# Kernel optimization log

Hardware: AMD Instinct MI355X
Metric: run time of the kernel (lower is better)

## Reference

```python
import jax, jax.numpy as jnp
import numpy as np

# Module hyperparameters (init_kwargs)
OUTLINER_RATIO = 0.01
SUB_RATIO = 0.2
SUB_BIT = 8
RANK = 16


def setup_inputs() -> dict:
    key = jax.random.key(0)
    x = jax.random.normal(key, (8, 2048, 4096), dtype=jnp.float32)
    return {"x": x}


def _lowrank_approx(A, q, key):
    """Randomized rank-q approximation of A (torch.svd_lowrank style, niter=2).
    A: [N, D]. Returns Q @ (Q^T A), a rank-q approximation of A."""
    n = A.shape[1]
    omega = jax.random.normal(key, (n, q), dtype=A.dtype)
    Q, _ = jnp.linalg.qr(A @ omega)            # [N, q]
    for _ in range(2):                          # power iterations
        Q2, _ = jnp.linalg.qr(A.T @ Q)          # [D, q]
        Q, _ = jnp.linalg.qr(A @ Q2)            # [N, q]
    return Q @ (Q.T @ A)                        # [N, D], rank q


def _get_statistics(x):
    """Outlier threshold (1-ratio quantile of |x[0]|), top-norm column list,
    and per-tensor symmetric quantization scale for the sub-outlier columns."""
    ax0 = jnp.abs(x[0]).ravel()
    k = int(ax0.shape[0] * (1.0 - OUTLINER_RATIO))      # kthvalue, 1-indexed
    outliner = jnp.sort(ax0)[k - 1]
    col_norm = jnp.mean(jnp.abs(x), axis=(0, 1))        # [D] per-column mean |x|
    kcols = int(x.shape[-1] * SUB_RATIO)
    _, cols = jax.lax.top_k(col_norm, kcols)            # sub-outlier column ids
    col_mask = jnp.zeros((x.shape[-1],), bool).at[cols].set(True)
    x_rem = jnp.where(jnp.abs(x) > outliner, 0.0, x)    # remove outliers
    x_sub = jnp.where(col_mask, x_rem, 0.0)
    qmax = float(2 ** (SUB_BIT - 1) - 1)
    scale = jnp.max(jnp.abs(x_sub)) / qmax
    return outliner, cols, scale


def _compress(x, outliner, cols, scale):
    """fake_divide_outliner_suboutlinear_svd: split x into outliers (kept exact),
    sub-outlier columns (fake-quantized to SUB_BIT bits), and a rank-RANK
    approximation of the remainder; recombine."""
    shape = x.shape
    D = shape[-1]
    x_out = jnp.where(jnp.abs(x) > outliner, x, 0.0)
    x_rem = x - x_out
    col_mask = jnp.zeros((D,), bool).at[cols].set(True)
    x_sub = jnp.where(col_mask, x_rem, 0.0)
    x_rem2 = x_rem - x_sub
    qmax = 2 ** (SUB_BIT - 1) - 1
    x_sub_q = jnp.clip(jnp.round(x_sub / scale), -qmax - 1, qmax) * scale
    x_lr = _lowrank_approx(x_rem2.reshape(-1, D), RANK, jax.random.key(42))
    return x_lr.reshape(shape) + x_out + x_sub_q


def reference(x):
    # forward output of the module is exact-erf GELU (F.gelu default)
    result = jax.nn.gelu(x, approximate=False)
    # iteration=0 < 10: compute statistics and the compressed activation
    # that would be saved for backward (this is the custom-kernel-heavy path).
    outliner, cols, scale = _get_statistics(x)
    x_compressed = _compress(x, outliner, cols, scale)
    return result, x_compressed, outliner, scale
```

## Files before the change

kernel.cpp:

```cpp
#include <hip/hip_runtime.h>
#include <math.h>

#define D_   4096
#define N_   16384
#define TOT  67108864ULL
#define KSEL 8304721u

__device__ unsigned long long g_colsum[D_];
__device__ unsigned int  g_hist[2048];
__device__ unsigned int  g_state[2];
__device__ float         g_outliner;
__device__ unsigned int  g_maxbits;
__device__ float         g_scale;
__device__ unsigned char g_mask[D_];
__device__ float g_omega[D_ * 16];
__device__ float g_tall [N_ * 16];
__device__ float g_small[D_ * 16];
__device__ float g_part [16777216];
__device__ float g_gpart[256 * 256];
__device__ float g_M[256];

__device__ __forceinline__ unsigned rotl32(unsigned v, int s) { return (v << s) | (v >> (32 - s)); }

__device__ __forceinline__ float erfinv32(float xx) {
  float w = -log1pf(-xx * xx);
  float p;
  if (w < 5.f) {
    w -= 2.5f;
    p = 2.81022636e-08f;
    p = fmaf(p, w, 3.43273939e-07f);
    p = fmaf(p, w, -3.5233877e-06f);
    p = fmaf(p, w, -4.39150654e-06f);
    p = fmaf(p, w, 0.00021858087f);
    p = fmaf(p, w, -0.00125372503f);
    p = fmaf(p, w, -0.00417768164f);
    p = fmaf(p, w, 0.246640727f);
    p = fmaf(p, w, 1.50140941f);
  } else {
    w = sqrtf(w) - 3.f;
    p = -0.000200214257f;
    p = fmaf(p, w, 0.000100950558f);
    p = fmaf(p, w, 0.00134934322f);
    p = fmaf(p, w, -0.00367342844f);
    p = fmaf(p, w, 0.00573950773f);
    p = fmaf(p, w, -0.0076224613f);
    p = fmaf(p, w, 0.00943887047f);
    p = fmaf(p, w, 1.00167406f);
    p = fmaf(p, w, 2.83297682f);
  }
  return p * xx;
}

__device__ __forceinline__ float bits_to_normal(unsigned b) {
  float f = __uint_as_float((b >> 9) | 0x3f800000u) - 1.0f;
  float u = fmaf(f, 2.0f, -0.99999994f);
  u = fmaxf(-0.99999994f, u);
  return 1.41421356f * erfinv32(u);
}

__device__ __forceinline__ float gelu_exact(float v) {
  return 0.5f * v * (1.f + erff(v * 0.70710678f));
}

__global__ void k_init() {
  int t = threadIdx.x;
  for (int i = t; i < D_; i += 256) g_colsum[i] = 0ull;
  for (int i = t; i < 2048; i += 256) g_hist[i] = 0u;
  if (t == 0) { g_state[0] = KSEL; g_state[1] = 0u; g_maxbits = 0u; }
}

__global__ __launch_bounds__(256) void k_pass1(const float* __restrict__ x, float* __restrict__ out0) {
  __shared__ unsigned lh[4 * 2056];
  int t = threadIdx.x, b = blockIdx.x;
  bool doh = (b < 64);
  for (int i = t; i < 4 * 2056; i += 256) lh[i] = 0u;
  int cp = (t >> 6) * 2056;
  float acc[16];
#pragma unroll
  for (int j = 0; j < 16; ++j) acc[j] = 0.f;
  __syncthreads();
  const float4* xv = (const float4*)(x + (size_t)b * 131072);
  float4* ov = (float4*)(out0 + (size_t)b * 131072);
  for (int i = 0; i < 128; i += 4) {
#pragma unroll
    for (int jj = 0; jj < 4; ++jj) {
      int f = t + 256 * (i + jj);
      float4 v = xv[f];
      float4 g;
      g.x = gelu_exact(v.x); g.y = gelu_exact(v.y); g.z = gelu_exact(v.z); g.w = gelu_exact(v.w);
      ov[f] = g;
      acc[jj * 4 + 0] += fabsf(v.x);
      acc[jj * 4 + 1] += fabsf(v.y);
      acc[jj * 4 + 2] += fabsf(v.z);
      acc[jj * 4 + 3] += fabsf(v.w);
      if (doh) {
        atomicAdd(&lh[cp + ((__float_as_uint(v.x) & 0x7fffffffu) >> 21)], 1u);
        atomicAdd(&lh[cp + ((__float_as_uint(v.y) & 0x7fffffffu) >> 21)], 1u);
        atomicAdd(&lh[cp + ((__float_as_uint(v.z) & 0x7fffffffu) >> 21)], 1u);
        atomicAdd(&lh[cp + ((__float_as_uint(v.w) & 0x7fffffffu) >> 21)], 1u);
      }
    }
  }
#pragma unroll
  for (int jj = 0; jj < 4; ++jj) {
    int c4 = t + 256 * jj;
#pragma unroll
    for (int k = 0; k < 4; ++k) {
      unsigned long long q = (unsigned long long)((double)acc[jj * 4 + k] * 4294967296.0 + 0.5);
      atomicAdd(&g_colsum[4 * c4 + k], q);
    }
  }
  if (doh) {
    __syncthreads();
    for (int i = t; i < 2048; i += 256) {
      unsigned c = lh[i] + lh[2056 + i] + lh[4112 + i] + lh[6168 + i];
      if (c) atomicAdd(&g_hist[i], c);
    }
  }
}

__global__ __launch_bounds__(256) void k_histL(const float* __restrict__ x, int level) {
  __shared__ unsigned lh[2048];
  int t = threadIdx.x, b = blockIdx.x;
  for (int i = t; i < 2048; i += 256) lh[i] = 0u;
  __syncthreads();
  unsigned pre = g_state[1];
  const float4* xv = (const float4*)x;
  size_t base = (size_t)b * 16384;
  for (int i = 0; i < 64; ++i) {
    float4 v = xv[base + t + 256 * i];
    unsigned u;
#define HPROC(comp) \
    u = __float_as_uint(comp) & 0x7fffffffu; \
    if (level == 1) { if ((u >> 21) == (pre >> 21)) atomicAdd(&lh[(u >> 10) & 0x7ffu], 1u); } \
    else            { if ((u >> 10) == (pre >> 10)) atomicAdd(&lh[u & 0x3ffu], 1u); }
    HPROC(v.x) HPROC(v.y) HPROC(v.z) HPROC(v.w)
#undef HPROC
  }
  __syncthreads();
  for (int i = t; i < 2048; i += 256) { unsigned c = lh[i]; if (c) atomicAdd(&g_hist[i], c); }
}

__global__ void k_scan(int level, float* __restrict__ od) {
  __shared__ unsigned h[2048];
  __shared__ unsigned ps[256];
  int t = threadIdx.x;
  unsigned loc = 0;
#pragma unroll
  for (int i = 0; i < 8; ++i) { unsigned v = g_hist[t * 8 + i]; h[t * 8 + i] = v; loc += v; }
  ps[t] = loc;
  __syncthreads();
  if (t == 0) {
    unsigned krem = g_state[0], pre = g_state[1];
    unsigned cum = 0; int g = 0;
    for (; g < 255; ++g) { if (cum + ps[g] >= krem) break; cum += ps[g]; }
    int b = g * 8;
    for (; b < 2047; ++b) { if (cum + h[b] >= krem) break; cum += h[b]; }
    krem -= cum;
    if (level == 0)      pre = ((unsigned)b) << 21;
    else if (level == 1) pre |= ((unsigned)b) << 10;
    else { pre |= (unsigned)b; g_outliner = __uint_as_float(pre); od[0] = __uint_as_float(pre); }
    g_state[0] = krem; g_state[1] = pre;
  }
  __syncthreads();
  for (int i = t; i < 2048; i += 256) g_hist[i] = 0u;
}

__global__ __launch_bounds__(1024) void k_colsel() {
  __shared__ unsigned long long s[4096];
  int t = threadIdx.x;
  for (int m = 0; m < 4; ++m) s[t + 1024 * m] = g_colsum[t + 1024 * m];
  __syncthreads();
  for (int k = 2; k <= 4096; k <<= 1) {
    for (int j = k >> 1; j > 0; j >>= 1) {
#pragma unroll
      for (int m = 0; m < 4; ++m) {
        int i = t + 1024 * m;
        int l = i ^ j;
        if (l > i) {
          unsigned long long a = s[i], c = s[l];
          bool up = ((i & k) == 0);
          if (up ? (a > c) : (a < c)) { s[i] = c; s[l] = a; }
        }
      }
      __syncthreads();
    }
  }
  unsigned long long T = s[4096 - 819];
  for (int m = 0; m < 4; ++m) { int i = t + 1024 * m; g_mask[i] = (g_colsum[i] >= T) ? 1 : 0; }
}

__global__ void k_omega() {
  unsigned i = blockIdx.x * 256 + threadIdx.x;
  if (i >= 65536u) return;
  const unsigned ks0 = 0u, ks1 = 42u, ks2 = 0x1BD11BDAu ^ 42u;
  unsigned x0 = 0u + ks0;
  unsigned x1 = i  + ks1;
#define RND(r) { x0 += x1; x1 = rotl32(x1, r); x1 ^= x0; }
  RND(13) RND(15) RND(26) RND(6)   x0 += ks1; x1 += ks2 + 1u;
  RND(17) RND(29) RND(16) RND(24)  x0 += ks2; x1 += ks0 + 2u;
  RND(13) RND(15) RND(26) RND(6)   x0 += ks0; x1 += ks1 + 3u;
  RND(17) RND(29) RND(16) RND(24)  x0 += ks1; x1 += ks2 + 4u;
  RND(13) RND(15) RND(26) RND(6)   x0 += ks2; x1 += ks0 + 5u;
#undef RND
  g_omega[i] = bits_to_normal(x0 ^ x1);
}

__global__ __launch_bounds__(256) void k_AB(const float* __restrict__ x, int bsel) {
  __shared__ float xt[256 * 33];
  int t = threadIdx.x;
  int rb = blockIdx.x, ks = blockIdx.y;
  const float* Bm = bsel ? g_small : g_omega;
  float thr = g_outliner;
  float acc[16];
#pragma unroll
  for (int q = 0; q < 16; ++q) acc[q] = 0.f;
  int row0 = rb * 256;
  for (int ch = 0; ch < 8; ++ch) {
    int d0 = ks * 256 + ch * 32;
#pragma unroll
    for (int m = 0; m < 8; ++m) {
      int f = t + 256 * m;
      int r = f >> 3, c4 = f & 7;
      float4 v = *(const float4*)(x + (size_t)(row0 + r) * D_ + d0 + 4 * c4);
      uchar4 mk = *(const uchar4*)(g_mask + d0 + 4 * c4);
      float a0 = (mk.x || fabsf(v.x) > thr) ? 0.f : v.x;
      float a1 = (mk.y || fabsf(v.y) > thr) ? 0.f : v.y;
      float a2 = (mk.z || fabsf(v.z) > thr) ? 0.f : v.z;
      float a3 = (mk.w || fabsf(v.w) > thr) ? 0.f : v.w;
      int base = r * 33 + 4 * c4;
      xt[base + 0] = a0; xt[base + 1] = a1; xt[base + 2] = a2; xt[base + 3] = a3;
    }
    __syncthreads();
    for (int d = 0; d < 32; ++d) {
      const float* br = Bm + (size_t)(d0 + d) * 16;
      float a0 = xt[t * 33 + d];
#pragma unroll
      for (int q = 0; q < 16; ++q) acc[q] = fmaf(a0, br[q], acc[q]);
    }
    __syncthreads();
  }
  float* p0 = g_part + ((size_t)ks * N_ + row0 + t) * 16;
#pragma unroll
  for (int q4 = 0; q4 < 4; ++q4)
    *(float4*)(p0 + 4 * q4) = make_float4(acc[4*q4], acc[4*q4+1], acc[4*q4+2], acc[4*q4+3]);
}

__global__ __launch_bounds__(1024) void k_AtB(const float* __restrict__ x, int do_max) {
  __shared__ float wm[16];
  int t = threadIdx.x, b = blockIdx.x;
  float thr = g_outliner;
  uchar4 mk = *(const uchar4*)(g_mask + 4 * t);
  float acc[4][16];
#pragma unroll
  for (int j = 0; j < 4; ++j)
#pragma unroll
    for (int q = 0; q < 16; ++q) acc[j][q] = 0.f;
  float mx = 0.f;
  size_t row0 = (size_t)b * 64;
  for (int r = 0; r < 64; ++r) {
    size_t row = row0 + r;
    float4 v = *(const float4*)(x + row * D_ + 4 * t);
    const float* br = g_tall + row * 16;
    float ax = fabsf(v.x), ay = fabsf(v.y), az = fabsf(v.z), aw = fabsf(v.w);
    float a0 = (mk.x || ax > thr) ? 0.f : v.x;
    float a1 = (mk.y || ay > thr) ? 0.f : v.y;
    float a2 = (mk.z || az > thr) ? 0.f : v.z;
    float a3 = (mk.w || aw > thr) ? 0.f : v.w;
    if (do_max) {
      if (mk.x && ax <= thr) mx = fmaxf(mx, ax);
      if (mk.y && ay <= thr) mx = fmaxf(mx, ay);
      if (mk.z && az <= thr) mx = fmaxf(mx, az);
      if (mk.w && aw <= thr) mx = fmaxf(mx, aw);
    }
#pragma unroll
    for (int q = 0; q < 16; ++q) {
      float bq = br[q];
      acc[0][q] = fmaf(a0, bq, acc[0][q]);
      acc[1][q] = fmaf(a1, bq, acc[1][q]);
      acc[2][q] = fmaf(a2, bq, acc[2][q]);
      acc[3][q] = fmaf(a3, bq, acc[3][q]);
    }
  }
  float* pb = g_part + ((size_t)b * D_ + 4 * t) * 16;
#pragma unroll
  for (int j = 0; j < 4; ++j)
#pragma unroll
    for (int q4 = 0; q4 < 4; ++q4)
      *(float4*)(pb + j * 16 + 4 * q4) =
        make_float4(acc[j][4*q4], acc[j][4*q4+1], acc[j][4*q4+2], acc[j][4*q4+3]);
  if (do_max) {
#pragma unroll
    for (int off = 32; off > 0; off >>= 1) mx = fmaxf(mx, __shfl_xor(mx, off, 64));
    if ((t & 63) == 0) wm[t >> 6] = mx;
    __syncthreads();
    if (t == 0) {
      float m2 = wm[0];
      for (int i = 1; i < 16; ++i) m2 = fmaxf(m2, wm[i]);
      atomicMax(&g_maxbits, __float_as_uint(m2));
    }
  }
}

__global__ __launch_bounds__(256) void k_combG0() {
  __shared__ float ys[1024];
  int t = threadIdx.x, blk = blockIdx.x;
#pragma unroll
  for (int m = 0; m < 4; ++m) {
    int j = blk * 1024 + m * 256 + t;
    float s = 0.f;
    for (int k2 = 0; k2 < 16; ++k2) s += g_part[k2 * 262144 + j];
    g_tall[j] = s;
    ys[m * 256 + t] = s;
  }
  __syncthreads();
  int a = t >> 4, b = t & 15;
  float acc = 0.f;
  for (int r = 0; r < 64; ++r) acc = fmaf(ys[r * 16 + a], ys[r * 16 + b], acc);
  g_gpart[blk * 256 + t] = acc;
}

__global__ __launch_bounds__(256) void k_combG1(int do_scale, float* __restrict__ od) {
  __shared__ float ys[256];
  int t = threadIdx.x, blk = blockIdx.x;
  int j = blk * 256 + t;
  float s = 0.f;
  for (int k2 = 0; k2 < 256; ++k2) s += g_part[k2 * 65536 + j];
  g_small[j] = s;
  ys[t] = s;
  if (do_scale && blk == 0 && t == 0) {
    float sc = __uint_as_float(g_maxbits) / 127.0f;
    g_scale = sc; od[0] = sc;
  }
  __syncthreads();
  int a = t >> 4, b = t & 15;
  float acc = 0.f;
  for (int r = 0; r < 16; ++r) acc = fmaf(ys[r * 16 + a], ys[r * 16 + b], acc);
  g_gpart[blk * 256 + t] = acc;
}

__global__ void k_chol(int mode) {
  __shared__ double G[256], L[256], M[256];
  int t = threadIdx.x;
  double s = 0.0;
  for (int p = 0; p < 256; ++p) s += (double)g_gpart[p * 256 + t];
  G[t] = s; M[t] = 0.0; L[t] = 0.0;
  __syncthreads();
  for (int j = 0; j < 16; ++j) {
    if (t == j) {
      double d = G[j * 16 + j];
      for (int k = 0; k < j; ++k) d -= L[j * 16 + k] * L[j * 16 + k];
      L[j * 16 + j] = sqrt(d);
    }
    __syncthreads();
    if (t > j && t < 16) {
      double d = G[t * 16 + j];
      for (int k = 0; k < j; ++k) d -= L[t * 16 + k] * L[j * 16 + k];
      L[t * 16 + j] = d / L[j * 16 + j];
    }
    __syncthreads();
  }
  if (t < 16) {
    int jc = t;
    M[jc * 16 + jc] = 1.0 / L[jc * 16 + jc];
    for (int i2 = jc + 1; i2 < 16; ++i2) {
      double s2 = 0.0;
      for (int k = jc; k < i2; ++k) s2 += L[i2 * 16 + k] * M[k * 16 + jc];
      M[i2 * 16 + jc] = -s2 / L[i2 * 16 + i2];
    }
  }
  __syncthreads();
  if (mode == 0) g_M[t] = (float)M[t];
  else {
    int i2 = t >> 4, j2 = t & 15;
    double s2 = 0.0;
    for (int k = 0; k < 16; ++k) s2 += M[k * 16 + i2] * M[k * 16 + j2];
    g_M[t] = (float)s2;
  }
}

__global__ __launch_bounds__(256) void k_scaleQ(int which) {
  __shared__ float Mf[256];
  float* Y = which ? g_small : g_tall;
  int t = threadIdx.x;
  Mf[t] = g_M[t];
  __syncthreads();
  size_t row = (size_t)blockIdx.x * 256 + t;
  float4* yr = (float4*)(Y + row * 16);
  float4 v0 = yr[0], v1 = yr[1], v2 = yr[2], v3 = yr[3];
  float y[16] = {v0.x,v0.y,v0.z,v0.w, v1.x,v1.y,v1.z,v1.w, v2.x,v2.y,v2.z,v2.w, v3.x,v3.y,v3.z,v3.w};
  float q[16];
#pragma unroll
  for (int jq = 0; jq < 16; ++jq) {
    float s = 0.f;
    for (int iq = 0; iq <= jq; ++iq) s = fmaf(Mf[jq * 16 + iq], y[iq], s);
    q[jq] = s;
  }
  yr[0] = make_float4(q[0],q[1],q[2],q[3]);
  yr[1] = make_float4(q[4],q[5],q[6],q[7]);
  yr[2] = make_float4(q[8],q[9],q[10],q[11]);
  yr[3] = make_float4(q[12],q[13],q[14],q[15]);
}

__global__ __launch_bounds__(256) void k_Zsolve() {
  __shared__ float Gf[256];
  int t = threadIdx.x;
  Gf[t] = g_M[t];
  __syncthreads();
  size_t d = (size_t)blockIdx.x * 256 + t;
  float4* wr = (float4*)(g_small + d * 16);
  float4 v0 = wr[0], v1 = wr[1], v2 = wr[2], v3 = wr[3];
  float w[16] = {v0.x,v0.y,v0.z,v0.w, v1.x,v1.y,v1.z,v1.w, v2.x,v2.y,v2.z,v2.w, v3.x,v3.y,v3.z,v3.w};
  float z[16];
#pragma unroll
  for (int jq = 0; jq < 16; ++jq) {
    float s = 0.f;
#pragma unroll
    for (int iq = 0; iq < 16; ++iq) s = fmaf(Gf[jq * 16 + iq], w[iq], s);
    z[jq] = s;
  }
  wr[0] = make_float4(z[0],z[1],z[2],z[3]);
  wr[1] = make_float4(z[4],z[5],z[6],z[7]);
  wr[2] = make_float4(z[8],z[9],z[10],z[11]);
  wr[3] = make_float4(z[12],z[13],z[14],z[15]);
}

__global__ __launch_bounds__(256) void k_final(const float* __restrict__ x, float* __restrict__ out1) {
  __shared__ float zt[16 * 516];
  int t = threadIdx.x;
  int rb = blockIdx.x, pn = blockIdx.y;
  int d0 = pn * 512;
  int row0 = rb * 256;
#pragma unroll
  for (int i = 0; i < 8; ++i) {
    int f = t + 256 * i;
    int dd = f >> 2, q4 = f & 3;
    float4 zv = *(const float4*)(g_small + (size_t)(d0 + dd) * 16 + 4 * q4);
    zt[(4 * q4 + 0) * 516 + dd] = zv.x;
    zt[(4 * q4 + 1) * 516 + dd] = zv.y;
    zt[(4 * q4 + 2) * 516 + dd] = zv.z;
    zt[(4 * q4 + 3) * 516 + dd] = zv.w;
  }
  __syncthreads();
  float thr = g_outliner, sc = g_scale;
  int lf = t & 127;
  int half = t >> 7;
  int dl = 4 * lf;
  float4 zq[16];
#pragma unroll
  for (int q = 0; q < 16; ++q) zq[q] = *(const float4*)&zt[q * 516 + dl];
  uchar4 mk = *(const uchar4*)(g_mask + d0 + dl);
  for (int i = 0; i < 128; ++i) {
    int row = row0 + 2 * i + half;
    int rowu = __builtin_amdgcn_readfirstlane(row);
    const float* yr = g_tall + (size_t)rowu * 16;
    float4 v = *(const float4*)(x + (size_t)rowu * D_ + d0 + dl);
    float4 a = make_float4(0.f, 0.f, 0.f, 0.f);
#pragma unroll
    for (int q = 0; q < 16; ++q) {
      float yq = yr[q];
      a.x = fmaf(yq, zq[q].x, a.x); a.y = fmaf(yq, zq[q].y, a.y);
      a.z = fmaf(yq, zq[q].z, a.z); a.w = fmaf(yq, zq[q].w, a.w);
    }
    float4 o;
    o.x = a.x + (fabsf(v.x) > thr ? v.x : (mk.x ? fminf(fmaxf(rintf(v.x / sc), -128.f), 127.f) * sc : 0.f));
    o.y = a.y + (fabsf(v.y) > thr ? v.y : (mk.y ? fminf(fmaxf(rintf(v.y / sc), -128.f), 127.f) * sc : 0.f));
    o.z = a.z + (fabsf(v.z) > thr ? v.z : (mk.z ? fminf(fmaxf(rintf(v.z / sc), -128.f), 127.f) * sc : 0.f));
    o.w = a.w + (fabsf(v.w) > thr ? v.w : (mk.w ? fminf(fmaxf(rintf(v.w / sc), -128.f), 127.f) * sc : 0.f));
    *(float4*)(out1 + (size_t)rowu * D_ + d0 + dl) = o;
  }
}

extern "C" void kernel_launch(void* const* d_in, const int* in_sizes, int n_in,
                              void* d_out, int out_size, void* d_ws, size_t ws_size,
                              hipStream_t stream) {
  (void)in_sizes; (void)n_in; (void)out_size; (void)d_ws; (void)ws_size;
  const float* x = (const float*)d_in[0];
  float* out = (float*)d_out;
  float* out0    = out;
  float* out1    = out + TOT;
  float* o_outl  = out + 2 * TOT;
  float* o_scale = out + 2 * TOT + 1;

  hipLaunchKernelGGL(k_init,  dim3(1),   dim3(256), 0, stream);
  hipLaunchKernelGGL(k_pass1, dim3(512), dim3(256), 0, stream, x, out0);
  hipLaunchKernelGGL(k_scan,  dim3(1),   dim3(256), 0, stream, 0, o_outl);
  hipLaunchKernelGGL(k_histL, dim3(128), dim3(256), 0, stream, x, 1);
  hipLaunchKernelGGL(k_scan,  dim3(1),   dim3(256), 0, stream, 1, o_outl);
  hipLaunchKernelGGL(k_histL, dim3(128), dim3(256), 0, stream, x, 2);
  hipLaunchKernelGGL(k_scan,  dim3(1),   dim3(256), 0, stream, 2, o_outl);
  hipLaunchKernelGGL(k_colsel, dim3(1),  dim3(1024), 0, stream);
  hipLaunchKernelGGL(k_omega, dim3(256), dim3(256), 0, stream);
  hipLaunchKernelGGL(k_AB,     dim3(64, 16), dim3(256), 0, stream, x, 0);
  hipLaunchKernelGGL(k_combG0, dim3(256),    dim3(256), 0, stream);
  hipLaunchKernelGGL(k_chol,   dim3(1),      dim3(256), 0, stream, 0);
  hipLaunchKernelGGL(k_scaleQ, dim3(64),     dim3(256), 0, stream, 0);
  hipLaunchKernelGGL(k_AtB,    dim3(256), dim3(1024), 0, stream, x, 1);
  hipLaunchKernelGGL(k_combG1, dim3(256), dim3(256),  0, stream, 1, o_scale);
  hipLaunchKernelGGL(k_chol,   dim3(1),   dim3(256),  0, stream, 0);
  hipLaunchKernelGGL(k_scaleQ, dim3(16),  dim3(256),  0, stream, 1);
  hipLaunchKernelGGL(k_AB,     dim3(64, 16), dim3(256), 0, stream, x, 1);
  hipLaunchKernelGGL(k_combG0, dim3(256),    dim3(256), 0, stream);
  hipLaunchKernelGGL(k_chol,   dim3(1),      dim3(256), 0, stream, 0);
  hipLaunchKernelGGL(k_scaleQ, dim3(64),     dim3(256), 0, stream, 0);
  hipLaunchKernelGGL(k_AtB,    dim3(256), dim3(1024), 0, stream, x, 0);
  hipLaunchKernelGGL(k_combG1, dim3(256), dim3(256),  0, stream, 0, o_scale);
  hipLaunchKernelGGL(k_chol,   dim3(1),   dim3(256),  0, stream, 0);
  hipLaunchKernelGGL(k_scaleQ, dim3(16),  dim3(256),  0, stream, 1);
  hipLaunchKernelGGL(k_AB,     dim3(64, 16), dim3(256), 0, stream, x, 1);
  hipLaunchKernelGGL(k_combG0, dim3(256),    dim3(256), 0, stream);
  hipLaunchKernelGGL(k_chol,   dim3(1),      dim3(256), 0, stream, 1);
  hipLaunchKernelGGL(k_AtB,    dim3(256), dim3(1024), 0, stream, x, 0);
  hipLaunchKernelGGL(k_combG1, dim3(256), dim3(256),  0, stream, 0, o_scale);
  hipLaunchKernelGGL(k_Zsolve, dim3(16),  dim3(256),  0, stream);
  hipLaunchKernelGGL(k_final,  dim3(64, 8), dim3(256), 0, stream, x, out1);
}
```

Baseline: 1.086 ms.

## Cache masked residual matrix in fp16 for power-iteration passes

The first A·omega pass now writes the masked residual (outliers and sub-outlier columns zeroed) as an fp16 copy. Every later A·B and Aᵀ·B pass reads that half-size buffer instead of re-reading fp32 x and re-applying the mask. The sub-outlier max reduction moves into the first pass, and the scale is written in the following combine kernel. This halves the bytes read in six of the seven large streaming passes, at the cost of an extra 128MB write and fp16 rounding of the residual fed into the low-rank factorisation.

```diff
diff --git a/kernel.cpp b/kernel.cpp
--- a/kernel.cpp
+++ b/kernel.cpp
@@ -1,4 +1,5 @@
 #include <hip/hip_runtime.h>
+#include <hip/hip_fp16.h>
 #include <math.h>
 
 #define D_   4096
@@ -13,6 +14,7 @@
 __device__ unsigned int  g_maxbits;
 __device__ float         g_scale;
 __device__ unsigned char g_mask[D_];
+__device__ __half g_af16[N_ * (size_t)D_];
 __device__ float g_omega[D_ * 16];
 __device__ float g_tall [N_ * 16];
 __device__ float g_small[D_ * 16];
@@ -206,30 +208,60 @@
   g_omega[i] = bits_to_normal(x0 ^ x1);
 }
 
-__global__ __launch_bounds__(256) void k_AB(const float* __restrict__ x, int bsel) {
+__global__ __launch_bounds__(256) void k_AB(const float* __restrict__ x, int bsel, int stage1) {
   __shared__ float xt[256 * 33];
   int t = threadIdx.x;
   int rb = blockIdx.x, ks = blockIdx.y;
   const float* Bm = bsel ? g_small : g_omega;
   float thr = g_outliner;
+  float mx = 0.f;
   float acc[16];
 #pragma unroll
   for (int q = 0; q < 16; ++q) acc[q] = 0.f;
   int row0 = rb * 256;
   for (int ch = 0; ch < 8; ++ch) {
     int d0 = ks * 256 + ch * 32;
-#pragma unroll
-    for (int m = 0; m < 8; ++m) {
-      int f = t + 256 * m;
-      int r = f >> 3, c4 = f & 7;
-      float4 v = *(const float4*)(x + (size_t)(row0 + r) * D_ + d0 + 4 * c4);
-      uchar4 mk = *(const uchar4*)(g_mask + d0 + 4 * c4);
-      float a0 = (mk.x || fabsf(v.x) > thr) ? 0.f : v.x;
-      float a1 = (mk.y || fabsf(v.y) > thr) ? 0.f : v.y;
-      float a2 = (mk.z || fabsf(v.z) > thr) ? 0.f : v.z;
-      float a3 = (mk.w || fabsf(v.w) > thr) ? 0.f : v.w;
-      int base = r * 33 + 4 * c4;
-      xt[base + 0] = a0; xt[base + 1] = a1; xt[base + 2] = a2; xt[base + 3] = a3;
+    if (stage1) {
+#pragma unroll
+      for (int m = 0; m < 8; ++m) {
+        int f = t + 256 * m;
+        int r = f >> 3, c4 = f & 7;
+        size_t off = (size_t)(row0 + r) * D_ + d0 + 4 * c4;
+        float4 v = *(const float4*)(x + off);
+        uchar4 mk = *(const uchar4*)(g_mask + d0 + 4 * c4);
+        float ax = fabsf(v.x), ay = fabsf(v.y), az = fabsf(v.z), aw = fabsf(v.w);
+        float a0 = (mk.x || ax > thr) ? 0.f : v.x;
+        float a1 = (mk.y || ay > thr) ? 0.f : v.y;
+        float a2 = (mk.z || az > thr) ? 0.f : v.z;
+        float a3 = (mk.w || aw > thr) ? 0.f : v.w;
+        if (mk.x && ax <= thr) mx = fmaxf(mx, ax);
+        if (mk.y && ay <= thr) mx = fmaxf(mx, ay);
+        if (mk.z && az <= thr) mx = fmaxf(mx, az);
+        if (mk.w && aw <= thr) mx = fmaxf(mx, aw);
+        union { __half2 h2[2]; uint2 u; } pk;
+        pk.h2[0] = __floats2half2_rn(a0, a1);
+        pk.h2[1] = __floats2half2_rn(a2, a3);
+        *(uint2*)(&g_af16[off]) = pk.u;
+        int base = r * 33 + 4 * c4;
+        xt[base + 0] = a0; xt[base + 1] = a1; xt[base + 2] = a2; xt[base + 3] = a3;
+      }
+    } else {
+#pragma unroll
+      for (int m = 0; m < 4; ++m) {
+        int f = t + 256 * m;
+        int r = f >> 2, c8 = f & 3;
+        size_t off = (size_t)(row0 + r) * D_ + d0 + 8 * c8;
+        uint4 raw = *(const uint4*)(&g_af16[off]);
+        float2 f0 = __half22float2(*(__half2*)&raw.x);
+        float2 f1 = __half22float2(*(__half2*)&raw.y);
+        float2 f2 = __half22float2(*(__half2*)&raw.z);
+        float2 f3 = __half22float2(*(__half2*)&raw.w);
+        int base = r * 33 + 8 * c8;
+        xt[base + 0] = f0.x; xt[base + 1] = f0.y;
+        xt[base + 2] = f1.x; xt[base + 3] = f1.y;
+        xt[base + 4] = f2.x; xt[base + 5] = f2.y;
+        xt[base + 6] = f3.x; xt[base + 7] = f3.y;
+      }
     }
     __syncthreads();
     for (int d = 0; d < 32; ++d) {
@@ -244,42 +276,34 @@
 #pragma unroll
   for (int q4 = 0; q4 < 4; ++q4)
     *(float4*)(p0 + 4 * q4) = make_float4(acc[4*q4], acc[4*q4+1], acc[4*q4+2], acc[4*q4+3]);
-}
-
-__global__ __launch_bounds__(1024) void k_AtB(const float* __restrict__ x, int do_max) {
-  __shared__ float wm[16];
+  if (stage1) {
+#pragma unroll
+    for (int off = 32; off > 0; off >>= 1) mx = fmaxf(mx, __shfl_xor(mx, off, 64));
+    if ((t & 63) == 0) atomicMax(&g_maxbits, __float_as_uint(mx));
+  }
+}
+
+__global__ __launch_bounds__(1024) void k_AtB() {
   int t = threadIdx.x, b = blockIdx.x;
-  float thr = g_outliner;
-  uchar4 mk = *(const uchar4*)(g_mask + 4 * t);
   float acc[4][16];
 #pragma unroll
   for (int j = 0; j < 4; ++j)
 #pragma unroll
     for (int q = 0; q < 16; ++q) acc[j][q] = 0.f;
-  float mx = 0.f;
   size_t row0 = (size_t)b * 64;
   for (int r = 0; r < 64; ++r) {
     size_t row = row0 + r;
-    float4 v = *(const float4*)(x + row * D_ + 4 * t);
+    uint2 raw = *(const uint2*)(&g_af16[row * D_ + 4 * t]);
+    float2 f01 = __half22float2(*(__half2*)&raw.x);
+    float2 f23 = __half22float2(*(__half2*)&raw.y);
     const float* br = g_tall + row * 16;
-    float ax = fabsf(v.x), ay = fabsf(v.y), az = fabsf(v.z), aw = fabsf(v.w);
-    float a0 = (mk.x || ax > thr) ? 0.f : v.x;
-    float a1 = (mk.y || ay > thr) ? 0.f : v.y;
-    float a2 = (mk.z || az > thr) ? 0.f : v.z;
-    float a3 = (mk.w || aw > thr) ? 0.f : v.w;
-    if (do_max) {
-      if (mk.x && ax <= thr) mx = fmaxf(mx, ax);
-      if (mk.y && ay <= thr) mx = fmaxf(mx, ay);
-      if (mk.z && az <= thr) mx = fmaxf(mx, az);
-      if (mk.w && aw <= thr) mx = fmaxf(mx, aw);
-    }
 #pragma unroll
     for (int q = 0; q < 16; ++q) {
       float bq = br[q];
-      acc[0][q] = fmaf(a0, bq, acc[0][q]);
-      acc[1][q] = fmaf(a1, bq, acc[1][q]);
-      acc[2][q] = fmaf(a2, bq, acc[2][q]);
-      acc[3][q] = fmaf(a3, bq, acc[3][q]);
+      acc[0][q] = fmaf(f01.x, bq, acc[0][q]);
+      acc[1][q] = fmaf(f01.y, bq, acc[1][q]);
+      acc[2][q] = fmaf(f23.x, bq, acc[2][q]);
+      acc[3][q] = fmaf(f23.y, bq, acc[3][q]);
     }
   }
   float* pb = g_part + ((size_t)b * D_ + 4 * t) * 16;
@@ -289,22 +313,15 @@
     for (int q4 = 0; q4 < 4; ++q4)
       *(float4*)(pb + j * 16 + 4 * q4) =
         make_float4(acc[j][4*q4], acc[j][4*q4+1], acc[j][4*q4+2], acc[j][4*q4+3]);
-  if (do_max) {
-#pragma unroll
-    for (int off = 32; off > 0; off >>= 1) mx = fmaxf(mx, __shfl_xor(mx, off, 64));
-    if ((t & 63) == 0) wm[t >> 6] = mx;
-    __syncthreads();
-    if (t == 0) {
-      float m2 = wm[0];
-      for (int i = 1; i < 16; ++i) m2 = fmaxf(m2, wm[i]);
-      atomicMax(&g_maxbits, __float_as_uint(m2));
-    }
-  }
-}
-
-__global__ __launch_bounds__(256) void k_combG0() {
+}
+
+__global__ __launch_bounds__(256) void k_combG0(int do_scale, float* __restrict__ od) {
   __shared__ float ys[1024];
   int t = threadIdx.x, blk = blockIdx.x;
+  if (do_scale && blk == 0 && t == 0) {
+    float sc = __uint_as_float(g_maxbits) / 127.0f;
+    g_scale = sc; od[0] = sc;
+  }
 #pragma unroll
   for (int m = 0; m < 4; ++m) {
     int j = blk * 1024 + m * 256 + t;
@@ -320,7 +337,7 @@
   g_gpart[blk * 256 + t] = acc;
 }
 
-__global__ __launch_bounds__(256) void k_combG1(int do_scale, float* __restrict__ od) {
+__global__ __launch_bounds__(256) void k_combG1() {
   __shared__ float ys[256];
   int t = threadIdx.x, blk = blockIdx.x;
   int j = blk * 256 + t;
@@ -328,10 +345,6 @@
   for (int k2 = 0; k2 < 256; ++k2) s += g_part[k2 * 65536 + j];
   g_small[j] = s;
   ys[t] = s;
-  if (do_scale && blk == 0 && t == 0) {
-    float sc = __uint_as_float(g_maxbits) / 127.0f;
-    g_scale = sc; od[0] = sc;
-  }
   __syncthreads();
   int a = t >> 4, b = t & 15;
   float acc = 0.f;
@@ -491,27 +504,27 @@
   hipLaunchKernelGGL(k_scan,  dim3(1),   dim3(256), 0, stream, 2, o_outl);
   hipLaunchKernelGGL(k_colsel, dim3(1),  dim3(1024), 0, stream);
   hipLaunchKernelGGL(k_omega, dim3(256), dim3(256), 0, stream);
-  hipLaunchKernelGGL(k_AB,     dim3(64, 16), dim3(256), 0, stream, x, 0);
-  hipLaunchKernelGGL(k_combG0, dim3(256),    dim3(256), 0, stream);
+  hipLaunchKernelGGL(k_AB,     dim3(64, 16), dim3(256), 0, stream, x, 0, 1);
+  hipLaunchKernelGGL(k_combG0, dim3(256),    dim3(256), 0, stream, 1, o_scale);
   hipLaunchKernelGGL(k_chol,   dim3(1),      dim3(256), 0, stream, 0);
   hipLaunchKernelGGL(k_scaleQ, dim3(64),     dim3(256), 0, stream, 0);
-  hipLaunchKernelGGL(k_AtB,    dim3(256), dim3(1024), 0, stream, x, 1);
-  hipLaunchKernelGGL(k_combG1, dim3(256), dim3(256),  0, stream, 1, o_scale);
+  hipLaunchKernelGGL(k_AtB,    dim3(256), dim3(1024), 0, stream);
+  hipLaunchKernelGGL(k_combG1, dim3(256), dim3(256),  0, stream);
   hipLaunchKernelGGL(k_chol,   dim3(1),   dim3(256),  0, stream, 0);
   hipLaunchKernelGGL(k_scaleQ, dim3(16),  dim3(256),  0, stream, 1);
-  hipLaunchKernelGGL(k_AB,     dim3(64, 16), dim3(256), 0, stream, x, 1);
-  hipLaunchKernelGGL(k_combG0, dim3(256),    dim3(256), 0, stream);
+  hipLaunchKernelGGL(k_AB,     dim3(64, 16), dim3(256), 0, stream, x, 1, 0);
+  hipLaunchKernelGGL(k_combG0, dim3(256),    dim3(256), 0, stream, 0, o_scale);
   hipLaunchKernelGGL(k_chol,   dim3(1),      dim3(256), 0, stream, 0);
   hipLaunchKernelGGL(k_scaleQ, dim3(64),     dim3(256), 0, stream, 0);
-  hipLaunchKernelGGL(k_AtB,    dim3(256), dim3(1024), 0, stream, x, 0);
-  hipLaunchKernelGGL(k_combG1, dim3(256), dim3(256),  0, stream, 0, o_scale);
+  hipLaunchKernelGGL(k_AtB,    dim3(256), dim3(1024), 0, stream);
+  hipLaunchKernelGGL(k_combG1, dim3(256), dim3(256),  0, stream);
   hipLaunchKernelGGL(k_chol,   dim3(1),   dim3(256),  0, stream, 0);
   hipLaunchKernelGGL(k_scaleQ, dim3(16),  dim3(256),  0, stream, 1);
-  hipLaunchKernelGGL(k_AB,     dim3(64, 16), dim3(256), 0, stream, x, 1);
-  hipLaunchKernelGGL(k_combG0, dim3(256),    dim3(256), 0, stream);
+  hipLaunchKernelGGL(k_AB,     dim3(64, 16), dim3(256), 0, stream, x, 1, 0);
+  hipLaunchKernelGGL(k_combG0, dim3(256),    dim3(256), 0, stream, 0, o_scale);
   hipLaunchKernelGGL(k_chol,   dim3(1),      dim3(256), 0, stream, 1);
-  hipLaunchKernelGGL(k_AtB,    dim3(256), dim3(1024), 0, stream, x, 0);
-  hipLaunchKernelGGL(k_combG1, dim3(256), dim3(256),  0, stream, 0, o_scale);
+  hipLaunchKernelGGL(k_AtB,    dim3(256), dim3(1024), 0, stream);
+  hipLaunchKernelGGL(k_combG1, dim3(256), dim3(256),  0, stream);
   hipLaunchKernelGGL(k_Zsolve, dim3(16),  dim3(256),  0, stream);
   hipLaunchKernelGGL(k_final,  dim3(64, 8), dim3(256), 0, stream, x, out1);
 }
```

New measurement: 1.123 ms. 3.4% more time.

## Fuse small reduction, Cholesky and scaling kernels using grid-wide atomic barriers

Applied to the files above, without the earlier changes.

Merges the column-combine, Gram, Cholesky, Q-scaling and Z-solve launches into the AB and AtB follow-up kernels, using software grid barriers built on global atomic counters. The omega RNG generation moves into otherwise idle pass1 blocks. The goal is to remove roughly twenty tiny serial kernel launches and their launch gaps. The software barriers need all 256 blocks to be resident at once; if they are not, the kernel can deadlock. The Cholesky also runs on a single block while the other blocks spin.

```diff
diff --git a/kernel.cpp b/kernel.cpp
--- a/kernel.cpp
+++ b/kernel.cpp
@@ -9,6 +9,7 @@
 __device__ unsigned long long g_colsum[D_];
 __device__ unsigned int  g_hist[2048];
 __device__ unsigned int  g_state[2];
+__device__ unsigned int  g_sync[16];
 __device__ float         g_outliner;
 __device__ unsigned int  g_maxbits;
 __device__ float         g_scale;
@@ -62,10 +63,68 @@
   return 0.5f * v * (1.f + erff(v * 0.70710678f));
 }
 
+__device__ __forceinline__ void gbar(int sid, unsigned target, bool wait) {
+  __syncthreads();
+  if (threadIdx.x == 0) {
+    __threadfence();
+    atomicAdd(&g_sync[sid], 1u);
+    if (wait) {
+      while (__hip_atomic_load(&g_sync[sid], __ATOMIC_ACQUIRE, __HIP_MEMORY_SCOPE_AGENT) < target)
+        __builtin_amdgcn_s_sleep(2);
+      __threadfence();
+    }
+  }
+  __syncthreads();
+}
+
+__device__ void chol16_block(int t, int mode) {
+  __shared__ double G[256], L[256], M[256];
+  if (t < 256) {
+    double s = 0.0;
+    for (int p = 0; p < 256; ++p) s += (double)g_gpart[p * 256 + t];
+    G[t] = s; L[t] = 0.0; M[t] = 0.0;
+  }
+  __syncthreads();
+  for (int j = 0; j < 16; ++j) {
+    if (t == j) {
+      double d = G[j * 16 + j];
+      for (int k = 0; k < j; ++k) d -= L[j * 16 + k] * L[j * 16 + k];
+      L[j * 16 + j] = sqrt(d);
+    }
+    __syncthreads();
+    if (t > j && t < 16) {
+      double d = G[t * 16 + j];
+      for (int k = 0; k < j; ++k) d -= L[t * 16 + k] * L[j * 16 + k];
+      L[t * 16 + j] = d / L[j * 16 + j];
+    }
+    __syncthreads();
+  }
+  if (t < 16) {
+    int jc = t;
+    M[jc * 16 + jc] = 1.0 / L[jc * 16 + jc];
+    for (int i2 = jc + 1; i2 < 16; ++i2) {
+      double s2 = 0.0;
+      for (int k = jc; k < i2; ++k) s2 += L[i2 * 16 + k] * M[k * 16 + jc];
+      M[i2 * 16 + jc] = -s2 / L[i2 * 16 + i2];
+    }
+  }
+  __syncthreads();
+  if (t < 256) {
+    if (mode == 0) g_M[t] = (float)M[t];
+    else {
+      int i2 = t >> 4, j2 = t & 15;
+      double s2 = 0.0;
+      for (int k = 0; k < 16; ++k) s2 += M[k * 16 + i2] * M[k * 16 + j2];
+      g_M[t] = (float)s2;
+    }
+  }
+}
+
 __global__ void k_init() {
   int t = threadIdx.x;
   for (int i = t; i < D_; i += 256) g_colsum[i] = 0ull;
   for (int i = t; i < 2048; i += 256) g_hist[i] = 0u;
+  if (t < 16) g_sync[t] = 0u;
   if (t == 0) { g_state[0] = KSEL; g_state[1] = 0u; g_maxbits = 0u; }
 }
 
@@ -79,6 +138,20 @@
 #pragma unroll
   for (int j = 0; j < 16; ++j) acc[j] = 0.f;
   __syncthreads();
+  if (b >= 64 && b < 320) {
+    unsigned i = (unsigned)(b - 64) * 256u + (unsigned)t;
+    const unsigned ks0 = 0u, ks1 = 42u, ks2 = 0x1BD11BDAu ^ 42u;
+    unsigned x0 = 0u + ks0;
+    unsigned x1 = i  + ks1;
+#define RND(r) { x0 += x1; x1 = rotl32(x1, r); x1 ^= x0; }
+    RND(13) RND(15) RND(26) RND(6)   x0 += ks1; x1 += ks2 + 1u;
+    RND(17) RND(29) RND(16) RND(24)  x0 += ks2; x1 += ks0 + 2u;
+    RND(13) RND(15) RND(26) RND(6)   x0 += ks0; x1 += ks1 + 3u;
+    RND(17) RND(29) RND(16) RND(24)  x0 += ks1; x1 += ks2 + 4u;
+    RND(13) RND(15) RND(26) RND(6)   x0 += ks2; x1 += ks0 + 5u;
+#undef RND
+    g_omega[i] = bits_to_normal(x0 ^ x1);
+  }
   const float4* xv = (const float4*)(x + (size_t)b * 131072);
   float4* ov = (float4*)(out0 + (size_t)b * 131072);
   for (int i = 0; i < 128; i += 4) {
@@ -190,22 +263,6 @@
   for (int m = 0; m < 4; ++m) { int i = t + 1024 * m; g_mask[i] = (g_colsum[i] >= T) ? 1 : 0; }
 }
 
-__global__ void k_omega() {
-  unsigned i = blockIdx.x * 256 + threadIdx.x;
-  if (i >= 65536u) return;
-  const unsigned ks0 = 0u, ks1 = 42u, ks2 = 0x1BD11BDAu ^ 42u;
-  unsigned x0 = 0u + ks0;
-  unsigned x1 = i  + ks1;
-#define RND(r) { x0 += x1; x1 = rotl32(x1, r); x1 ^= x0; }
-  RND(13) RND(15) RND(26) RND(6)   x0 += ks1; x1 += ks2 + 1u;
-  RND(17) RND(29) RND(16) RND(24)  x0 += ks2; x1 += ks0 + 2u;
-  RND(13) RND(15) RND(26) RND(6)   x0 += ks0; x1 += ks1 + 3u;
-  RND(17) RND(29) RND(16) RND(24)  x0 += ks1; x1 += ks2 + 4u;
-  RND(13) RND(15) RND(26) RND(6)   x0 += ks2; x1 += ks0 + 5u;
-#undef RND
-  g_omega[i] = bits_to_normal(x0 ^ x1);
-}
-
 __global__ __launch_bounds__(256) void k_AB(const float* __restrict__ x, int bsel) {
   __shared__ float xt[256 * 33];
   int t = threadIdx.x;
@@ -246,8 +303,54 @@
     *(float4*)(p0 + 4 * q4) = make_float4(acc[4*q4], acc[4*q4+1], acc[4*q4+2], acc[4*q4+3]);
 }
 
-__global__ __launch_bounds__(1024) void k_AtB(const float* __restrict__ x, int do_max) {
-  __shared__ float wm[16];
+__global__ __launch_bounds__(256) void k_post0(int sid, int mode) {
+  __shared__ float ys[1024];
+  __shared__ float Mf[256];
+  int t = threadIdx.x, blk = blockIdx.x;
+#pragma unroll
+  for (int m = 0; m < 4; ++m) {
+    int j = blk * 1024 + m * 256 + t;
+    float s = 0.f;
+    for (int k2 = 0; k2 < 16; ++k2) s += g_part[k2 * 262144 + j];
+    g_tall[j] = s;
+    ys[m * 256 + t] = s;
+  }
+  __syncthreads();
+  {
+    int a = t >> 4, b = t & 15;
+    float acc = 0.f;
+    for (int r = 0; r < 64; ++r) acc = fmaf(ys[r * 16 + a], ys[r * 16 + b], acc);
+    g_gpart[blk * 256 + t] = acc;
+  }
+  gbar(sid, 256, mode == 0 || blk == 0);
+  if (blk == 0) chol16_block(t, mode);
+  if (mode == 0) {
+    gbar(sid + 1, 256, true);
+    Mf[t] = g_M[t];
+    __syncthreads();
+    if (t < 64) {
+      float y[16], q[16];
+#pragma unroll
+      for (int iq = 0; iq < 16; ++iq) y[iq] = ys[t * 16 + iq];
+#pragma unroll
+      for (int jq = 0; jq < 16; ++jq) {
+        float s = 0.f;
+        for (int iq = 0; iq <= jq; ++iq) s = fmaf(Mf[jq * 16 + iq], y[iq], s);
+        q[jq] = s;
+      }
+      float4* yr = (float4*)(g_tall + ((size_t)blk * 64 + t) * 16);
+      yr[0] = make_float4(q[0],q[1],q[2],q[3]);
+      yr[1] = make_float4(q[4],q[5],q[6],q[7]);
+      yr[2] = make_float4(q[8],q[9],q[10],q[11]);
+      yr[3] = make_float4(q[12],q[13],q[14],q[15]);
+    }
+  }
+}
+
+__global__ __launch_bounds__(1024) void k_AtB_f(const float* __restrict__ x, int sid,
+                                                int mode, int do_max, float* __restrict__ od) {
+  __shared__ float ys[256];
+  __shared__ float Mf[256];
   int t = threadIdx.x, b = blockIdx.x;
   float thr = g_outliner;
   uchar4 mk = *(const uchar4*)(g_mask + 4 * t);
@@ -292,137 +395,69 @@
   if (do_max) {
 #pragma unroll
     for (int off = 32; off > 0; off >>= 1) mx = fmaxf(mx, __shfl_xor(mx, off, 64));
-    if ((t & 63) == 0) wm[t >> 6] = mx;
-    __syncthreads();
-    if (t == 0) {
-      float m2 = wm[0];
-      for (int i = 1; i < 16; ++i) m2 = fmaxf(m2, wm[i]);
-      atomicMax(&g_maxbits, __float_as_uint(m2));
-    }
-  }
-}
-
-__global__ __launch_bounds__(256) void k_combG0() {
-  __shared__ float ys[1024];
-  int t = threadIdx.x, blk = blockIdx.x;
-#pragma unroll
-  for (int m = 0; m < 4; ++m) {
-    int j = blk * 1024 + m * 256 + t;
+    if ((t & 63) == 0) atomicMax(&g_maxbits, __float_as_uint(mx));
+  }
+  gbar(sid, 256, true);
+  if (t < 256) {
+    int j = b * 256 + t;
     float s = 0.f;
-    for (int k2 = 0; k2 < 16; ++k2) s += g_part[k2 * 262144 + j];
-    g_tall[j] = s;
-    ys[m * 256 + t] = s;
-  }
-  __syncthreads();
-  int a = t >> 4, b = t & 15;
-  float acc = 0.f;
-  for (int r = 0; r < 64; ++r) acc = fmaf(ys[r * 16 + a], ys[r * 16 + b], acc);
-  g_gpart[blk * 256 + t] = acc;
-}
-
-__global__ __launch_bounds__(256) void k_combG1(int do_scale, float* __restrict__ od) {
-  __shared__ float ys[256];
-  int t = threadIdx.x, blk = blockIdx.x;
-  int j = blk * 256 + t;
-  float s = 0.f;
-  for (int k2 = 0; k2 < 256; ++k2) s += g_part[k2 * 65536 + j];
-  g_small[j] = s;
-  ys[t] = s;
-  if (do_scale && blk == 0 && t == 0) {
-    float sc = __uint_as_float(g_maxbits) / 127.0f;
-    g_scale = sc; od[0] = sc;
-  }
-  __syncthreads();
-  int a = t >> 4, b = t & 15;
-  float acc = 0.f;
-  for (int r = 0; r < 16; ++r) acc = fmaf(ys[r * 16 + a], ys[r * 16 + b], acc);
-  g_gpart[blk * 256 + t] = acc;
-}
-
-__global__ void k_chol(int mode) {
-  __shared__ double G[256], L[256], M[256];
-  int t = threadIdx.x;
-  double s = 0.0;
-  for (int p = 0; p < 256; ++p) s += (double)g_gpart[p * 256 + t];
-  G[t] = s; M[t] = 0.0; L[t] = 0.0;
-  __syncthreads();
-  for (int j = 0; j < 16; ++j) {
-    if (t == j) {
-      double d = G[j * 16 + j];
-      for (int k = 0; k < j; ++k) d -= L[j * 16 + k] * L[j * 16 + k];
-      L[j * 16 + j] = sqrt(d);
-    }
-    __syncthreads();
-    if (t > j && t < 16) {
-      double d = G[t * 16 + j];
-      for (int k = 0; k < j; ++k) d -= L[t * 16 + k] * L[j * 16 + k];
-      L[t * 16 + j] = d / L[j * 16 + j];
-    }
-    __syncthreads();
-  }
-  if (t < 16) {
-    int jc = t;
-    M[jc * 16 + jc] = 1.0 / L[jc * 16 + jc];
-    for (int i2 = jc + 1; i2 < 16; ++i2) {
-      double s2 = 0.0;
-      for (int k = jc; k < i2; ++k) s2 += L[i2 * 16 + k] * M[k * 16 + jc];
-      M[i2 * 16 + jc] = -s2 / L[i2 * 16 + i2];
-    }
-  }
-  __syncthreads();
-  if (mode == 0) g_M[t] = (float)M[t];
-  else {
-    int i2 = t >> 4, j2 = t & 15;
-    double s2 = 0.0;
-    for (int k = 0; k < 16; ++k) s2 += M[k * 16 + i2] * M[k * 16 + j2];
-    g_M[t] = (float)s2;
-  }
-}
-
-__global__ __launch_bounds__(256) void k_scaleQ(int which) {
-  __shared__ float Mf[256];
-  float* Y = which ? g_small : g_tall;
-  int t = threadIdx.x;
-  Mf[t] = g_M[t];
-  __syncthreads();
-  size_t row = (size_t)blockIdx.x * 256 + t;
-  float4* yr = (float4*)(Y + row * 16);
-  float4 v0 = yr[0], v1 = yr[1], v2 = yr[2], v3 = yr[3];
-  float y[16] = {v0.x,v0.y,v0.z,v0.w, v1.x,v1.y,v1.z,v1.w, v2.x,v2.y,v2.z,v2.w, v3.x,v3.y,v3.z,v3.w};
-  float q[16];
-#pragma unroll
-  for (int jq = 0; jq < 16; ++jq) {
-    float s = 0.f;
-    for (int iq = 0; iq <= jq; ++iq) s = fmaf(Mf[jq * 16 + iq], y[iq], s);
-    q[jq] = s;
-  }
-  yr[0] = make_float4(q[0],q[1],q[2],q[3]);
-  yr[1] = make_float4(q[4],q[5],q[6],q[7]);
-  yr[2] = make_float4(q[8],q[9],q[10],q[11]);
-  yr[3] = make_float4(q[12],q[13],q[14],q[15]);
-}
-
-__global__ __launch_bounds__(256) void k_Zsolve() {
-  __shared__ float Gf[256];
-  int t = threadIdx.x;
-  Gf[t] = g_M[t];
-  __syncthreads();
-  size_t d = (size_t)blockIdx.x * 256 + t;
-  float4* wr = (float4*)(g_small + d * 16);
-  float4 v0 = wr[0], v1 = wr[1], v2 = wr[2], v3 = wr[3];
-  float w[16] = {v0.x,v0.y,v0.z,v0.w, v1.x,v1.y,v1.z,v1.w, v2.x,v2.y,v2.z,v2.w, v3.x,v3.y,v3.z,v3.w};
-  float z[16];
-#pragma unroll
-  for (int jq = 0; jq < 16; ++jq) {
-    float s = 0.f;
-#pragma unroll
-    for (int iq = 0; iq < 16; ++iq) s = fmaf(Gf[jq * 16 + iq], w[iq], s);
-    z[jq] = s;
-  }
-  wr[0] = make_float4(z[0],z[1],z[2],z[3]);
-  wr[1] = make_float4(z[4],z[5],z[6],z[7]);
-  wr[2] = make_float4(z[8],z[9],z[10],z[11]);
-  wr[3] = make_float4(z[12],z[13],z[14],z[15]);
+    for (int k2 = 0; k2 < 256; ++k2) s += g_part[k2 * 65536 + j];
+    ys[t] = s;
+  }
+  __syncthreads();
+  if (mode == 0) {
+    if (do_max && b == 0 && t == 0) {
+      float sc = __uint_as_float(atomicMax(&g_maxbits, 0u)) / 127.0f;
+      g_scale = sc; od[0] = sc;
+    }
+    if (t < 256) {
+      int a = t >> 4, bb = t & 15;
+      float acc2 = 0.f;
+      for (int r = 0; r < 16; ++r) acc2 = fmaf(ys[r * 16 + a], ys[r * 16 + bb], acc2);
+      g_gpart[b * 256 + t] = acc2;
+    }
+    gbar(sid + 1, 256, true);
+    if (b == 0) chol16_block(t, 0);
+    gbar(sid + 2, 256, true);
+    if (t < 256) Mf[t] = g_M[t];
+    __syncthreads();
+    if (t < 16) {
+      float y[16], q[16];
+#pragma unroll
+      for (int iq = 0; iq < 16; ++iq) y[iq] = ys[t * 16 + iq];
+#pragma unroll
+      for (int jq = 0; jq < 16; ++jq) {
+        float s = 0.f;
+        for (int iq = 0; iq <= jq; ++iq) s = fmaf(Mf[jq * 16 + iq], y[iq], s);
+        q[jq] = s;
+      }
+      float4* yr = (float4*)(g_small + ((size_t)b * 16 + t) * 16);
+      yr[0] = make_float4(q[0],q[1],q[2],q[3]);
+      yr[1] = make_float4(q[4],q[5],q[6],q[7]);
+      yr[2] = make_float4(q[8],q[9],q[10],q[11]);
+      yr[3] = make_float4(q[12],q[13],q[14],q[15]);
+    }
+  } else {
+    if (t < 256) Mf[t] = g_M[t];
+    __syncthreads();
+    if (t < 16) {
+      float w[16], z[16];
+#pragma unroll
+      for (int iq = 0; iq < 16; ++iq) w[iq] = ys[t * 16 + iq];
+#pragma unroll
+      for (int jq = 0; jq < 16; ++jq) {
+        float s = 0.f;
+#pragma unroll
+        for (int iq = 0; iq < 16; ++iq) s = fmaf(Mf[jq * 16 + iq], w[iq], s);
+        z[jq] = s;
+      }
+      float4* wr = (float4*)(g_small + ((size_t)b * 16 + t) * 16);
+      wr[0] = make_float4(z[0],z[1],z[2],z[3]);
+      wr[1] = make_float4(z[4],z[5],z[6],z[7]);
+      wr[2] = make_float4(z[8],z[9],z[10],z[11]);
+      wr[3] = make_float4(z[12],z[13],z[14],z[15]);
+    }
+  }
 }
 
 __global__ __launch_bounds__(256) void k_final(const float* __restrict__ x, float* __restrict__ out1) {
@@ -490,28 +525,14 @@
   hipLaunchKernelGGL(k_histL, dim3(128), dim3(256), 0, stream, x, 2);
   hipLaunchKernelGGL(k_scan,  dim3(1),   dim3(256), 0, stream, 2, o_outl);
   hipLaunchKernelGGL(k_colsel, dim3(1),  dim3(1024), 0, stream);
-  hipLaunchKernelGGL(k_omega, dim3(256), dim3(256), 0, stream);
   hipLaunchKernelGGL(k_AB,     dim3(64, 16), dim3(256), 0, stream, x, 0);
-  hipLaunchKernelGGL(k_combG0, dim3(256),    dim3(256), 0, stream);
-  hipLaunchKernelGGL(k_chol,   dim3(1),      dim3(256), 0, stream, 0);
-  hipLaunchKernelGGL(k_scaleQ, dim3(64),     dim3(256), 0, stream, 0);
-  hipLaunchKernelGGL(k_AtB,    dim3(256), dim3(1024), 0, stream, x, 1);
-  hipLaunchKernelGGL(k_combG1, dim3(256), dim3(256),  0, stream, 1, o_scale);
-  hipLaunchKernelGGL(k_chol,   dim3(1),   dim3(256),  0, stream, 0);
-  hipLaunchKernelGGL(k_scaleQ, dim3(16),  dim3(256),  0, stream, 1);
+  hipLaunchKernelGGL(k_post0,  dim3(256),    dim3(256), 0, stream, 0, 0);
+  hipLaunchKernelGGL(k_AtB_f,  dim3(256), dim3(1024), 0, stream, x, 2, 0, 1, o_scale);
   hipLaunchKernelGGL(k_AB,     dim3(64, 16), dim3(256), 0, stream, x, 1);
-  hipLaunchKernelGGL(k_combG0, dim3(256),    dim3(256), 0, stream);
-  hipLaunchKernelGGL(k_chol,   dim3(1),      dim3(256), 0, stream, 0);
-  hipLaunchKernelGGL(k_scaleQ, dim3(64),     dim3(256), 0, stream, 0);
-  hipLaunchKernelGGL(k_AtB,    dim3(256), dim3(1024), 0, stream, x, 0);
-  hipLaunchKernelGGL(k_combG1, dim3(256), dim3(256),  0, stream, 0, o_scale);
-  hipLaunchKernelGGL(k_chol,   dim3(1),   dim3(256),  0, stream, 0);
-  hipLaunchKernelGGL(k_scaleQ, dim3(16),  dim3(256),  0, stream, 1);
+  hipLaunchKernelGGL(k_post0,  dim3(256),    dim3(256), 0, stream, 5, 0);
+  hipLaunchKernelGGL(k_AtB_f,  dim3(256), dim3(1024), 0, stream, x, 7, 0, 0, o_scale);
   hipLaunchKernelGGL(k_AB,     dim3(64, 16), dim3(256), 0, stream, x, 1);
-  hipLaunchKernelGGL(k_combG0, dim3(256),    dim3(256), 0, stream);
-  hipLaunchKernelGGL(k_chol,   dim3(1),      dim3(256), 0, stream, 1);
-  hipLaunchKernelGGL(k_AtB,    dim3(256), dim3(1024), 0, stream, x, 0);
-  hipLaunchKernelGGL(k_combG1, dim3(256), dim3(256),  0, stream, 0, o_scale);
-  hipLaunchKernelGGL(k_Zsolve, dim3(16),  dim3(256),  0, stream);
+  hipLaunchKernelGGL(k_post0,  dim3(256),    dim3(256), 0, stream, 10, 1);
+  hipLaunchKernelGGL(k_AtB_f,  dim3(256), dim3(1024), 0, stream, x, 11, 1, 0, o_scale);
   hipLaunchKernelGGL(k_final,  dim3(64, 8), dim3(256), 0, stream, x, out1);
 }
```

After: 1.719 ms. 58.2% more time.

## Reduce AtB partials in-block to shrink split-K slices from 256 to 16

Applied to the files above, without the earlier changes.

k_AtB now tiles 256 columns by 1024 rows per block, with 16 row-waves whose partial 16-wide products are summed through shared memory before being written. This cuts g_part partials from 256 slices to 16, so k_combG1 reads far less global memory. The combine loops are unrolled with four independent accumulators. The cost is a 64KB shared buffer per block, which limits occupancy, extra barriers, and a per-wave atomicMax instead of one per block.

```diff
diff --git a/kernel.cpp b/kernel.cpp
--- a/kernel.cpp
+++ b/kernel.cpp
@@ -247,20 +247,22 @@
 }
 
 __global__ __launch_bounds__(1024) void k_AtB(const float* __restrict__ x, int do_max) {
-  __shared__ float wm[16];
-  int t = threadIdx.x, b = blockIdx.x;
+  int t = threadIdx.x;
+  int cp = blockIdx.x, rg = blockIdx.y;
+  int c4 = t & 63, rw = t >> 6;
+  int col0 = cp * 256 + 4 * c4;
   float thr = g_outliner;
-  uchar4 mk = *(const uchar4*)(g_mask + 4 * t);
+  uchar4 mk = *(const uchar4*)(g_mask + col0);
   float acc[4][16];
 #pragma unroll
   for (int j = 0; j < 4; ++j)
 #pragma unroll
     for (int q = 0; q < 16; ++q) acc[j][q] = 0.f;
   float mx = 0.f;
-  size_t row0 = (size_t)b * 64;
-  for (int r = 0; r < 64; ++r) {
-    size_t row = row0 + r;
-    float4 v = *(const float4*)(x + row * D_ + 4 * t);
+  size_t rowbase = (size_t)rg * 1024 + rw;
+  for (int i = 0; i < 64; ++i) {
+    size_t row = rowbase + (size_t)i * 16;
+    float4 v = *(const float4*)(x + row * D_ + col0);
     const float* br = g_tall + row * 16;
     float ax = fabsf(v.x), ay = fabsf(v.y), az = fabsf(v.z), aw = fabsf(v.w);
     float a0 = (mk.x || ax > thr) ? 0.f : v.x;
@@ -282,23 +284,27 @@
       acc[3][q] = fmaf(a3, bq, acc[3][q]);
     }
   }
-  float* pb = g_part + ((size_t)b * D_ + 4 * t) * 16;
-#pragma unroll
-  for (int j = 0; j < 4; ++j)
+  __shared__ float red[16 * 1024];
+#pragma unroll
+  for (int j = 0; j < 4; ++j) {
+    float* rp = red + rw * 1024 + c4 * 16;
 #pragma unroll
     for (int q4 = 0; q4 < 4; ++q4)
-      *(float4*)(pb + j * 16 + 4 * q4) =
-        make_float4(acc[j][4*q4], acc[j][4*q4+1], acc[j][4*q4+2], acc[j][4*q4+3]);
+      *(float4*)(rp + 4 * q4) = make_float4(acc[j][4*q4], acc[j][4*q4+1], acc[j][4*q4+2], acc[j][4*q4+3]);
+    __syncthreads();
+    {
+      float s = 0.f;
+#pragma unroll 4
+      for (int k2 = 0; k2 < 16; ++k2) s += red[k2 * 1024 + t];
+      int cc = t >> 4, qq = t & 15;
+      g_part[((size_t)rg * 65536) + ((size_t)(cp * 256 + 4 * cc + j)) * 16 + qq] = s;
+    }
+    __syncthreads();
+  }
   if (do_max) {
 #pragma unroll
     for (int off = 32; off > 0; off >>= 1) mx = fmaxf(mx, __shfl_xor(mx, off, 64));
-    if ((t & 63) == 0) wm[t >> 6] = mx;
-    __syncthreads();
-    if (t == 0) {
-      float m2 = wm[0];
-      for (int i = 1; i < 16; ++i) m2 = fmaxf(m2, wm[i]);
-      atomicMax(&g_maxbits, __float_as_uint(m2));
-    }
+    if ((t & 63) == 0) atomicMax(&g_maxbits, __float_as_uint(mx));
   }
 }
 
@@ -308,8 +314,15 @@
 #pragma unroll
   for (int m = 0; m < 4; ++m) {
     int j = blk * 1024 + m * 256 + t;
-    float s = 0.f;
-    for (int k2 = 0; k2 < 16; ++k2) s += g_part[k2 * 262144 + j];
+    float s0 = 0.f, s1 = 0.f, s2 = 0.f, s3 = 0.f;
+#pragma unroll
+    for (int k2 = 0; k2 < 4; ++k2) {
+      s0 += g_part[(k2 * 4 + 0) * 262144 + j];
+      s1 += g_part[(k2 * 4 + 1) * 262144 + j];
+      s2 += g_part[(k2 * 4 + 2) * 262144 + j];
+      s3 += g_part[(k2 * 4 + 3) * 262144 + j];
+    }
+    float s = (s0 + s1) + (s2 + s3);
     g_tall[j] = s;
     ys[m * 256 + t] = s;
   }
@@ -324,8 +337,15 @@
   __shared__ float ys[256];
   int t = threadIdx.x, blk = blockIdx.x;
   int j = blk * 256 + t;
-  float s = 0.f;
-  for (int k2 = 0; k2 < 256; ++k2) s += g_part[k2 * 65536 + j];
+  float s0 = 0.f, s1 = 0.f, s2 = 0.f, s3 = 0.f;
+#pragma unroll
+  for (int k2 = 0; k2 < 4; ++k2) {
+    s0 += g_part[(size_t)(k2 * 4 + 0) * 65536 + j];
+    s1 += g_part[(size_t)(k2 * 4 + 1) * 65536 + j];
+    s2 += g_part[(size_t)(k2 * 4 + 2) * 65536 + j];
+    s3 += g_part[(size_t)(k2 * 4 + 3) * 65536 + j];
+  }
+  float s = (s0 + s1) + (s2 + s3);
   g_small[j] = s;
   ys[t] = s;
   if (do_scale && blk == 0 && t == 0) {
@@ -495,7 +515,7 @@
   hipLaunchKernelGGL(k_combG0, dim3(256),    dim3(256), 0, stream);
   hipLaunchKernelGGL(k_chol,   dim3(1),      dim3(256), 0, stream, 0);
   hipLaunchKernelGGL(k_scaleQ, dim3(64),     dim3(256), 0, stream, 0);
-  hipLaunchKernelGGL(k_AtB,    dim3(256), dim3(1024), 0, stream, x, 1);
+  hipLaunchKernelGGL(k_AtB,    dim3(16, 16), dim3(1024), 0, stream, x, 1);
   hipLaunchKernelGGL(k_combG1, dim3(256), dim3(256),  0, stream, 1, o_scale);
   hipLaunchKernelGGL(k_chol,   dim3(1),   dim3(256),  0, stream, 0);
   hipLaunchKernelGGL(k_scaleQ, dim3(16),  dim3(256),  0, stream, 1);
@@ -503,14 +523,14 @@
   hipLaunchKernelGGL(k_combG0, dim3(256),    dim3(256), 0, stream);
   hipLaunchKernelGGL(k_chol,   dim3(1),      dim3(256), 0, stream, 0);
   hipLaunchKernelGGL(k_scaleQ, dim3(64),     dim3(256), 0, stream, 0);
-  hipLaunchKernelGGL(k_AtB,    dim3(256), dim3(1024), 0, stream, x, 0);
+  hipLaunchKernelGGL(k_AtB,    dim3(16, 16), dim3(1024), 0, stream, x, 0);
   hipLaunchKernelGGL(k_combG1, dim3(256), dim3(256),  0, stream, 0, o_scale);
   hipLaunchKernelGGL(k_chol,   dim3(1),   dim3(256),  0, stream, 0);
   hipLaunchKernelGGL(k_scaleQ, dim3(16),  dim3(256),  0, stream, 1);
   hipLaunchKernelGGL(k_AB,     dim3(64, 16), dim3(256), 0, stream, x, 1);
   hipLaunchKernelGGL(k_combG0, dim3(256),    dim3(256), 0, stream);
   hipLaunchKernelGGL(k_chol,   dim3(1),      dim3(256), 0, stream, 1);
-  hipLaunchKernelGGL(k_AtB,    dim3(256), dim3(1024), 0, stream, x, 0);
+  hipLaunchKernelGGL(k_AtB,    dim3(16, 16), dim3(1024), 0, stream, x, 0);
   hipLaunchKernelGGL(k_combG1, dim3(256), dim3(256),  0, stream, 0, o_scale);
   hipLaunchKernelGGL(k_Zsolve, dim3(16),  dim3(256),  0, stream);
   hipLaunchKernelGGL(k_final,  dim3(64, 8), dim3(256), 0, stream, x, out1);
```

Result: slower. 1.258 ms (+15.8%).
